# Optimization experiments

Measured on AMD Instinct MI355X. Metric: run time of the kernel, lower is better.

Reference implementation:

```python
import jax, jax.numpy as jnp
import numpy as np
from jax import lax

B, C, H, W = 16, 384, 28, 28
HEADS = 8


def _ln(x, g, b):
    mu = jnp.mean(x, axis=-1, keepdims=True)
    var = jnp.var(x, axis=-1, keepdims=True)
    return (x - mu) * lax.rsqrt(var + 1e-5) * g + b


def setup_inputs() -> dict:
    key = jax.random.key(0)
    ks = jax.random.split(key, 8)
    s = 0.02
    return {
        "cls_token": jax.random.normal(ks[0], (B, 1, C), dtype=jnp.float32),
        "x": jax.random.normal(ks[1], (B, C, H, W), dtype=jnp.float32),
        "conv_w": jax.random.normal(ks[2], (C, 1, 3, 3), dtype=jnp.float32) * s,
        "conv_b": jnp.zeros((C,), jnp.float32),
        "ln1_g": jnp.ones((C,), jnp.float32),
        "ln1_b": jnp.zeros((C,), jnp.float32),
        "qkv_w": jax.random.normal(ks[3], (3 * C, C), dtype=jnp.float32) * s,
        "proj_w": jax.random.normal(ks[4], (C, C), dtype=jnp.float32) * s,
        "proj_b": jnp.zeros((C,), jnp.float32),
        "ln2_g": jnp.ones((C,), jnp.float32),
        "ln2_b": jnp.zeros((C,), jnp.float32),
        "fc1_w": jax.random.normal(ks[5], (4 * C, C), dtype=jnp.float32) * s,
        "fc1_b": jnp.zeros((4 * C,), jnp.float32),
        "fc2_w": jax.random.normal(ks[6], (C, 4 * C), dtype=jnp.float32) * s,
        "fc2_b": jnp.zeros((C,), jnp.float32),
    }


def reference(cls_token, x, conv_w, conv_b, ln1_g, ln1_b, qkv_w, proj_w, proj_b,
              ln2_g, ln2_b, fc1_w, fc1_b, fc2_w, fc2_b):
    Bv, Cv, Hv, Wv = x.shape
    h = HEADS
    d = Cv // h
    # depthwise 3x3 positional conv (groups=dim), residual add
    pe = lax.conv_general_dilated(
        x, conv_w, window_strides=(1, 1), padding="SAME",
        feature_group_count=Cv,
        dimension_numbers=("NCHW", "OIHW", "NCHW")) + conv_b[None, :, None, None]
    x = x + pe
    x_patch = x.reshape(Bv, Cv, Hv * Wv).transpose(0, 2, 1)  # [B, HW, C]
    xc = jnp.concatenate([cls_token, x_patch], axis=1)       # [B, N, C]
    N = xc.shape[1]

    # --- Attention with inline global_attn stats (first-call / int sentinel path) ---
    y = _ln(xc, ln1_g, ln1_b)
    qkv = (y @ qkv_w.T).reshape(Bv, N, 3, h, d)
    q = qkv[:, :, 0].transpose(0, 2, 1, 3)  # [B, h, N, d]
    k = qkv[:, :, 1].transpose(0, 2, 1, 3)
    v = qkv[:, :, 2].transpose(0, 2, 1, 3)
    scale = d ** -0.5
    attn = jax.nn.softmax(jnp.einsum("bhnd,bhmd->bhnm", q, k) * scale, axis=-1)
    # per-token global attention statistic: mean over heads of cls row (excl. cls)
    global_attn = jnp.mean(attn[:, :, 0, 1:], axis=1)  # [B, N-1]
    o = jnp.einsum("bhnm,bhmd->bhnd", attn, v).transpose(0, 2, 1, 3).reshape(Bv, N, Cv)
    xc = xc + (o @ proj_w.T + proj_b)

    # --- MLP (GELU exact, matching torch nn.GELU default) ---
    y2 = _ln(xc, ln2_g, ln2_b)
    m = jax.nn.gelu(y2 @ fc1_w.T + fc1_b, approximate=False) @ fc2_w.T + fc2_b
    xc = xc + m

    cls_out = xc[:, :1]                                            # [B, 1, C]
    x_out = xc[:, 1:].transpose(0, 2, 1).reshape(Bv, Cv, Hv, Wv)    # [B, C, H, W]
    return cls_out, x_out, global_attn
```

## Files before the change

### kernel.cpp

```cpp
#include <hip/hip_runtime.h>
#include <hip/hip_bf16.h>

#define DI __device__ __forceinline__

typedef __attribute__((ext_vector_type(4))) float f32x4;
typedef __attribute__((ext_vector_type(8))) short bf16x8;
typedef __attribute__((ext_vector_type(4))) short bf16x4;

static constexpr int CB = 16;
static constexpr int CC = 384;
static constexpr int CH = 28, CW = 28;
static constexpr int CD = 48;
static constexpr int CN = 785;
static constexpr int CM = CB * CN;
static constexpr int C3 = 3 * CC;
static constexpr int CF = 4 * CC;
static constexpr int HW = CH * CW;
static constexpr int NP = 832;

DI short f2b(float f) {
  __hip_bfloat16 h = __float2bfloat16(f);
  return *reinterpret_cast<short*>(&h);
}
DI float b2f(short s) {
  union { unsigned u; float f; } x;
  x.u = ((unsigned)(unsigned short)s) << 16;
  return x.f;
}

DI void gload16(const short* g, short* l) {
  __builtin_amdgcn_global_load_lds((const __attribute__((address_space(1))) void*)g,
                                   (__attribute__((address_space(3))) void*)l, 16, 0, 0);
}

__global__ void k_misc(const float* __restrict__ cls, float* __restrict__ xc,
                       float* __restrict__ ga) {
  const int gid = blockIdx.x * 256 + threadIdx.x;
  if (gid < CB * HW) ga[gid] = 0.f;
  if (gid < CB * CC) {
    const int b = gid / CC, c = gid % CC;
    xc[((size_t)b * CN) * CC + c] = cls[gid];
  }
}

__global__ void k_wconv(const float* __restrict__ s0, const float* __restrict__ s1,
                        const float* __restrict__ s2, const float* __restrict__ s3,
                        short* __restrict__ dst) {
  const int gid = (blockIdx.x * 256 + threadIdx.x) * 4;
  if (gid >= 1769472) return;
  const float* s; int off;
  if (gid < 442368)       { s = s0; off = gid; }
  else if (gid < 589824)  { s = s1; off = gid - 442368; }
  else if (gid < 1179648) { s = s2; off = gid - 589824; }
  else                    { s = s3; off = gid - 1179648; }
  f32x4 v = *(const f32x4*)(s + off);
  bf16x4 o;
#pragma unroll
  for (int i = 0; i < 4; i++) o[i] = f2b(v[i]);
  *(bf16x4*)(dst + gid) = o;
}

__global__ __launch_bounds__(256) void k_conv_t(const float* __restrict__ x,
                                                const float* __restrict__ cw,
                                                const float* __restrict__ cb,
                                                float* __restrict__ xc) {
  __shared__ float T[64][65];
  __shared__ float Wc[64 * 9];
  __shared__ float Cbs[64];
  const int b = blockIdx.z;
  const int cc = blockIdx.y * 64;
  const int hw0 = blockIdx.x * 64;
  const int t = threadIdx.x;
  const int hwi = t & 63, ci0 = t >> 6;
  const int hw = hw0 + hwi;
  const int yy = hw / CW, xx = hw % CW;
  const int ci2 = t & 63, hb2 = t >> 6;

  for (int i = t; i < 64 * 9; i += 256) Wc[i] = cw[cc * 9 + i];
  if (t < 64) Cbs[t] = cb[cc + t];
  __syncthreads();
  if (hw < HW) {
    const int ctr = yy * CW + xx;
    int off9[9]; float mk9[9];
#pragma unroll
    for (int ky = 0; ky < 3; ky++)
#pragma unroll
      for (int kx = 0; kx < 3; kx++) {
        const int iy = yy + ky - 1, ix = xx + kx - 1;
        const bool v = (iy >= 0 && iy < CH && ix >= 0 && ix < CW);
        off9[ky * 3 + kx] = v ? iy * CW + ix : ctr;
        mk9[ky * 3 + kx] = v ? 1.f : 0.f;
      }
#pragma unroll
    for (int j = 0; j < 16; j += 2) {
      const int cl0 = ci0 * 16 + j;
      const float* xp0 = x + ((size_t)(b * CC + cc + cl0)) * HW;
      const float* xp1 = xp0 + HW;
      float t0[9], t1[9];
#pragma unroll
      for (int q = 0; q < 9; q++) { t0[q] = xp0[off9[q]]; t1[q] = xp1[off9[q]]; }
      const float c0 = xp0[ctr], c1 = xp1[ctr];
      float a0 = Cbs[cl0], a1 = Cbs[cl0 + 1];
#pragma unroll
      for (int q = 0; q < 9; q++) {
        a0 += Wc[cl0 * 9 + q] * (t0[q] * mk9[q]);
        a1 += Wc[(cl0 + 1) * 9 + q] * (t1[q] * mk9[q]);
      }
      T[cl0][hwi] = c0 + a0;
      T[cl0 + 1][hwi] = c1 + a1;
    }
  }
  __syncthreads();
#pragma unroll
  for (int j = 0; j < 16; j++) {
    const int hwl = hb2 + j * 4;
    if (hw0 + hwl < HW)
      xc[((size_t)b * CN + 1 + hw0 + hwl) * CC + cc + ci2] = T[ci2][hwl];
  }
}

__global__ __launch_bounds__(256) void k_ln(const float* __restrict__ xin,
                                            const float* __restrict__ g,
                                            const float* __restrict__ bta,
                                            short* __restrict__ y, int Mtot) {
  const int row = blockIdx.x * 4 + (threadIdx.x >> 6);
  const int l = threadIdx.x & 63;
  if (row >= Mtot) return;
  const float* xr = xin + (size_t)row * CC;
  float v[6], s = 0.f, ss = 0.f;
#pragma unroll
  for (int i = 0; i < 6; i++) {
    v[i] = xr[l + i * 64];
    s += v[i];
    ss += v[i] * v[i];
  }
#pragma unroll
  for (int m = 1; m < 64; m <<= 1) { s += __shfl_xor(s, m); ss += __shfl_xor(ss, m); }
  const float mu = s * (1.f / CC);
  const float var = ss * (1.f / CC) - mu * mu;
  const float r = rsqrtf(var + 1e-5f);
#pragma unroll
  for (int i = 0; i < 6; i++) {
    const int c = l + i * 64;
    y[(size_t)row * CC + c] = f2b((v[i] - mu) * r * g[c] + bta[c]);
  }
}

template <int BM, int DOGELU, int DORES, int DOBIAS, int OUTBF>
__global__ __launch_bounds__(256) void k_gemm(const short* __restrict__ A,
                                              const short* __restrict__ W,
                                              const float* __restrict__ bias,
                                              const float* __restrict__ resid,
                                              void* __restrict__ out_,
                                              int M, int N, int K) {
  constexpr int MI = BM / 32;
  constexpr int ACALLS = BM / 64;
  constexpr int ASZ = BM * 32, BSZ = 128 * 32;
  __shared__ short As[3 * ASZ];
  __shared__ short Bs[3 * BSZ];
  const int bm = blockIdx.x * BM, bn = blockIdx.y * 128;
  const int t = threadIdx.x, w = t >> 6, l = t & 63, g = l >> 4, li = l & 15;
  const int wm = (w >> 1) * (BM / 2), wn = (w & 1) * 64;

  const int srow = l >> 2;
  const int scol = (l & 3) * 8;
  const short* aSrc[ACALLS]; int aOff[ACALLS];
#pragma unroll
  for (int j = 0; j < ACALLS; j++) {
    int arow = bm + w * (BM / 4) + j * 16 + srow; if (arow > M - 1) arow = M - 1;
    aSrc[j] = A + (size_t)arow * K + scol;
    aOff[j] = (w * (BM / 4) + j * 16) * 32;
  }
  const short* bSrc[2]; int bOff[2];
#pragma unroll
  for (int j = 0; j < 2; j++) {
    const int brow = bn + w * 32 + j * 16 + srow;
    bSrc[j] = W + (size_t)brow * K + scol;
    bOff[j] = (w * 32 + j * 16) * 32;
  }

  auto stage = [&](int buf, int kt) {
    const int ko = kt * 32;
#pragma unroll
    for (int j = 0; j < ACALLS; j++)
      gload16(aSrc[j] + ko, &As[buf * ASZ] + aOff[j]);
#pragma unroll
    for (int j = 0; j < 2; j++)
      gload16(bSrc[j] + ko, &Bs[buf * BSZ] + bOff[j]);
  };

  f32x4 acc[MI][4] = {};
  const int nkt = K / 32;
  stage(0, 0);
  stage(1, 1);
  int cur = 0;
  for (int kt = 0; kt < nkt; kt++) {
    if (kt + 2 < nkt) {
      int nb = cur + 2; if (nb >= 3) nb -= 3;
      stage(nb, kt + 2);
      if constexpr (BM == 128) asm volatile("s_waitcnt vmcnt(8)" ::: "memory");
      else                     asm volatile("s_waitcnt vmcnt(6)" ::: "memory");
    } else if (kt + 2 == nkt) {
      if constexpr (BM == 128) asm volatile("s_waitcnt vmcnt(4)" ::: "memory");
      else                     asm volatile("s_waitcnt vmcnt(3)" ::: "memory");
    } else {
      asm volatile("s_waitcnt vmcnt(0)" ::: "memory");
    }
    __builtin_amdgcn_sched_barrier(0);
    __builtin_amdgcn_s_barrier();

    const short* Ab = &As[cur * ASZ];
    const short* Bb = &Bs[cur * BSZ];
    bf16x8 af[MI], bf[4];
#pragma unroll
    for (int mi = 0; mi < MI; mi++)
      af[mi] = *(const bf16x8*)&Ab[(wm + mi * 16 + li) * 32 + g * 8];
#pragma unroll
    for (int ni = 0; ni < 4; ni++)
      bf[ni] = *(const bf16x8*)&Bb[(wn + ni * 16 + li) * 32 + g * 8];
#pragma unroll
    for (int mi = 0; mi < MI; mi++)
#pragma unroll
      for (int ni = 0; ni < 4; ni++)
        acc[mi][ni] = __builtin_amdgcn_mfma_f32_16x16x32_bf16(af[mi], bf[ni], acc[mi][ni], 0, 0, 0);

    asm volatile("s_waitcnt lgkmcnt(0)" ::: "memory");
    __builtin_amdgcn_sched_barrier(0);
    __builtin_amdgcn_s_barrier();
    cur = (cur == 2) ? 0 : cur + 1;
  }

#pragma unroll
  for (int mi = 0; mi < MI; mi++)
#pragma unroll
    for (int ni = 0; ni < 4; ni++) {
      const int col = bn + wn + ni * 16 + li;
      float bv = 0.f;
      if constexpr (DOBIAS) bv = bias[col];
#pragma unroll
      for (int r = 0; r < 4; r++) {
        const int row = bm + wm + mi * 16 + g * 4 + r;
        if (row < M) {
          float v = acc[mi][ni][r] + bv;
          if constexpr (DOGELU) v = 0.5f * v * (1.f + erff(v * 0.7071067811865475f));
          if constexpr (DORES) v += resid[(size_t)row * N + col];
          if constexpr (OUTBF)
            ((short*)out_)[(size_t)row * N + col] = f2b(v);
          else
            ((float*)out_)[(size_t)row * N + col] = v;
        }
      }
    }
}

__global__ __launch_bounds__(256) void k_vt(const short* __restrict__ qkv,
                                            short* __restrict__ vt) {
  __shared__ short Tl[48 * 71];
  const int n0 = blockIdx.x * 64;
  const int bh = blockIdx.y;
  const int b = bh >> 3, h = bh & 7;
  const int t = threadIdx.x;
  const size_t bbase = (size_t)b * CN;
#pragma unroll
  for (int it = 0; it < 2; it++) {
    const int gi = t + it * 256;
    if (gi < 384) {
      const int nrel = gi / 6, dg = gi % 6;
      const int n = n0 + nrel;
      bf16x8 val = {};
      if (n < CN)
        val = *(const bf16x8*)(qkv + (bbase + n) * C3 + 2 * CC + h * CD + dg * 8);
#pragma unroll
      for (int i = 0; i < 8; i++) Tl[(dg * 8 + i) * 71 + nrel] = val[i];
    }
  }
  __syncthreads();
#pragma unroll
  for (int it = 0; it < 2; it++) {
    const int gj = t + it * 256;
    if (gj < 384) {
      const int d = gj >> 3, ng = gj & 7;
      bf16x8 v;
#pragma unroll
      for (int i = 0; i < 8; i++) v[i] = Tl[d * 71 + ng * 8 + i];
      *(bf16x8*)(vt + ((size_t)bh * CD + d) * NP + n0 + ng * 8) = v;
    }
  }
}

__global__ __launch_bounds__(256) void k_attn(const short* __restrict__ qkv,
                                              const short* __restrict__ vt,
                                              short* __restrict__ o) {
  __shared__ short Ks[64 * 48];
  __shared__ short Vs[48 * 64];
  const int f = blockIdx.x;
  const int xslot = f & 7, grp = f >> 3;
  const int bh = xslot + 8 * (grp & 15);
  const int qt = grp >> 4;
  const int b = bh >> 3, h = bh & 7;
  const int q0 = qt * 64;
  const int t = threadIdx.x, w = t >> 6, l = t & 63, g = l >> 4, li = l & 15;
  const size_t bbase = (size_t)b * CN;

  const int qrow = q0 + w * 16 + li;
  const int qr = qrow > CN - 1 ? CN - 1 : qrow;
  const short* qb = qkv + (bbase + qr) * C3 + h * CD;
  bf16x8 qf0 = *(const bf16x8*)(qb + g * 8);
  bf16x8 qf1 = {};
  if (g < 2) qf1 = *(const bf16x8*)(qb + 32 + g * 8);

  float mr = -1e30f, ls = 0.f;
  f32x4 oa[3] = {};
  const float scale = 0.14433756729740643f;

  const int krow0 = t / 6, kcg0 = t % 6;
  const int krow1 = (t + 256) / 6, kcg1 = (t + 256) % 6;
  const int vd0 = t >> 3, vkvg0 = t & 7;
  const int vd1 = (t + 256) >> 3, vkvg1 = (t + 256) & 7;
  const short* kbase = qkv + bbase * C3 + CC + h * CD;
  const short* vbase = vt + (size_t)bh * CD * NP;

  bf16x8 kr0 = {}, kr1 = {}, vr0 = {}, vr1 = {};
  kr0 = *(const bf16x8*)(kbase + (size_t)min(krow0, CN - 1) * C3 + kcg0 * 8);
  vr0 = *(const bf16x8*)(vbase + vd0 * NP + vkvg0 * 8);
  if (t < 128) {
    kr1 = *(const bf16x8*)(kbase + (size_t)min(krow1, CN - 1) * C3 + kcg1 * 8);
    vr1 = *(const bf16x8*)(vbase + vd1 * NP + vkvg1 * 8);
  }

  for (int kt = 0; kt < 13; kt++) {
    const int kv0 = kt * 64;
    __syncthreads();
    *(bf16x8*)((char*)Ks + ((krow0 * 96 + kcg0 * 16) ^ ((krow0 & 7) << 4))) = kr0;
    *(bf16x8*)((char*)Vs + ((vd0 * 128 + vkvg0 * 16) ^ ((vd0 & 7) << 4))) = vr0;
    if (t < 128) {
      *(bf16x8*)((char*)Ks + ((krow1 * 96 + kcg1 * 16) ^ ((krow1 & 7) << 4))) = kr1;
      *(bf16x8*)((char*)Vs + ((vd1 * 128 + vkvg1 * 16) ^ ((vd1 & 7) << 4))) = vr1;
    }
    __syncthreads();
    if (kt < 12) {
      const int kn = kv0 + 64;
      kr0 = *(const bf16x8*)(kbase + (size_t)min(kn + krow0, CN - 1) * C3 + kcg0 * 8);
      vr0 = *(const bf16x8*)(vbase + vd0 * NP + kn + vkvg0 * 8);
      if (t < 128) {
        kr1 = *(const bf16x8*)(kbase + (size_t)min(kn + krow1, CN - 1) * C3 + kcg1 * 8);
        vr1 = *(const bf16x8*)(vbase + vd1 * NP + kn + vkvg1 * 8);
      }
    }

    f32x4 s[4];
    __builtin_amdgcn_s_setprio(1);
#pragma unroll
    for (int ni = 0; ni < 4; ni++) {
      const int krw = ni * 16 + li;
      const int sw = (krw & 7) << 4;
      bf16x8 kf0 = *(const bf16x8*)((char*)Ks + ((krw * 96 + g * 16) ^ sw));
      bf16x8 kf1 = {};
      if (g < 2) kf1 = *(const bf16x8*)((char*)Ks + ((krw * 96 + 64 + g * 16) ^ sw));
      f32x4 acc = {};
      acc = __builtin_amdgcn_mfma_f32_16x16x32_bf16(kf0, qf0, acc, 0, 0, 0);
      acc = __builtin_amdgcn_mfma_f32_16x16x32_bf16(kf1, qf1, acc, 0, 0, 0);
      s[ni] = acc;
    }
    __builtin_amdgcn_s_setprio(0);

    float mt = -1e30f;
#pragma unroll
    for (int ni = 0; ni < 4; ni++)
#pragma unroll
      for (int r = 0; r < 4; r++) {
        const int kva = kv0 + ni * 16 + g * 4 + r;
        const float v = (kva < CN) ? s[ni][r] * scale : -1e30f;
        s[ni][r] = v;
        mt = fmaxf(mt, v);
      }
    mt = fmaxf(mt, __shfl_xor(mt, 16));
    mt = fmaxf(mt, __shfl_xor(mt, 32));
    const float mn = fmaxf(mr, mt);
    const float al = __expf(mr - mn);
    mr = mn;
    float ps = 0.f;
#pragma unroll
    for (int ni = 0; ni < 4; ni++)
#pragma unroll
      for (int r = 0; r < 4; r++) {
        const float p = __expf(s[ni][r] - mn);
        s[ni][r] = p;
        ps += p;
      }
    ps += __shfl_xor(ps, 16);
    ps += __shfl_xor(ps, 32);
    ls = ls * al + ps;

    const int sb = (l & 48) + ((l & 48) >> 2);
    float ar[4];
#pragma unroll
    for (int r = 0; r < 4; r++) ar[r] = __shfl(al, sb + r);
#pragma unroll
    for (int d = 0; d < 3; d++)
#pragma unroll
      for (int r = 0; r < 4; r++) oa[d][r] *= ar[r];

    bf16x8 pa[2];
#pragma unroll
    for (int ks = 0; ks < 2; ks++)
#pragma unroll
      for (int i = 0; i < 8; i++)
        pa[ks][i] = f2b(i < 4 ? s[2 * ks][i] : s[2 * ks + 1][i - 4]);

    __builtin_amdgcn_s_setprio(1);
#pragma unroll
    for (int d = 0; d < 3; d++) {
      const int drow = d * 16 + li;
      const int sw = (drow & 7) << 4;
#pragma unroll
      for (int ks = 0; ks < 2; ks++) {
        bf16x4 lo = *(const bf16x4*)((char*)Vs + ((drow * 128 + ks * 64 + g * 8) ^ sw));
        bf16x4 hi = *(const bf16x4*)((char*)Vs + ((drow * 128 + ks * 64 + 32 + g * 8) ^ sw));
        bf16x8 vb;
#pragma unroll
        for (int i = 0; i < 4; i++) { vb[i] = lo[i]; vb[4 + i] = hi[i]; }
        oa[d] = __builtin_amdgcn_mfma_f32_16x16x32_bf16(pa[ks], vb, oa[d], 0, 0, 0);
      }
    }
    __builtin_amdgcn_s_setprio(0);
  }

  const int sb = (l & 48) + ((l & 48) >> 2);
  float lr[4];
#pragma unroll
  for (int r = 0; r < 4; r++) lr[r] = __shfl(ls, sb + r);
#pragma unroll
  for (int d = 0; d < 3; d++)
#pragma unroll
    for (int r = 0; r < 4; r++) {
      const int n = q0 + w * 16 + g * 4 + r;
      if (n < CN)
        o[(bbase + n) * CC + h * CD + d * 16 + li] = f2b(oa[d][r] / lr[r]);
    }
}

__global__ __launch_bounds__(256) void k_gattn(const short* __restrict__ qkv,
                                               float* __restrict__ ga) {
  const int b = blockIdx.x >> 3, h = blockIdx.x & 7;
  __shared__ float red[4];
  const int t = threadIdx.x;
  const size_t bbase = (size_t)b * CN;
  const short* q0 = qkv + bbase * C3 + h * CD;
  float qv[CD];
#pragma unroll
  for (int i = 0; i < CD; i++) qv[i] = b2f(q0[i]);
  float lg[4], ev[4];
  float lmax = -1e30f;
#pragma unroll
  for (int j = 0; j < 4; j++) {
    const int m = t + j * 256;
    if (m < CN) {
      const short* kr = qkv + (bbase + m) * C3 + CC + h * CD;
      float acc = 0.f;
#pragma unroll
      for (int i = 0; i < CD; i++) acc += qv[i] * b2f(kr[i]);
      lg[j] = acc * 0.14433756729740643f;
      lmax = fmaxf(lmax, lg[j]);
    } else lg[j] = -1e30f;
  }
  for (int msk = 1; msk < 64; msk <<= 1) lmax = fmaxf(lmax, __shfl_xor(lmax, msk));
  if ((t & 63) == 0) red[t >> 6] = lmax;
  __syncthreads();
  lmax = fmaxf(fmaxf(red[0], red[1]), fmaxf(red[2], red[3]));
  __syncthreads();
  float es = 0.f;
#pragma unroll
  for (int j = 0; j < 4; j++) {
    ev[j] = (t + j * 256 < CN) ? __expf(lg[j] - lmax) : 0.f;
    es += ev[j];
  }
  for (int msk = 1; msk < 64; msk <<= 1) es += __shfl_xor(es, msk);
  if ((t & 63) == 0) red[t >> 6] = es;
  __syncthreads();
  es = red[0] + red[1] + red[2] + red[3];
  const float inv = 0.125f / es;
#pragma unroll
  for (int j = 0; j < 4; j++) {
    const int m = t + j * 256;
    if (m >= 1 && m < CN) atomicAdd(&ga[b * HW + m - 1], ev[j] * inv);
  }
}

__global__ __launch_bounds__(256) void k_out(const float* __restrict__ xc,
                                             float* __restrict__ outp) {
  const int b = blockIdx.y, tile = blockIdx.x, t = threadIdx.x;
  if (tile == 78) {
    for (int i = t; i < CC; i += 256)
      outp[b * CC + i] = xc[((size_t)b * CN) * CC + i];
    return;
  }
  __shared__ float T[64][65];
  const int ct = tile / 13, ht = tile % 13;
  const int c0 = ct * 64, hw0 = ht * 64;
  const int ci = t & 63, hb = t >> 6;
  for (int j = 0; j < 16; j++) {
    const int hwl = hb + j * 4;
    if (hw0 + hwl < HW)
      T[ci][hwl] = xc[((size_t)b * CN + 1 + hw0 + hwl) * CC + c0 + ci];
  }
  __syncthreads();
  const int hi = t & 63, cb2 = t >> 6;
  float* xo = outp + CB * CC;
  for (int j = 0; j < 16; j++) {
    const int cl = cb2 + j * 4;
    if (hw0 + hi < HW)
      xo[((size_t)(b * CC + c0 + cl)) * HW + hw0 + hi] = T[cl][hi];
  }
}

extern "C" void kernel_launch(void* const* d_in, const int* in_sizes, int n_in,
                              void* d_out, int out_size, void* d_ws, size_t ws_size,
                              hipStream_t stream) {
  const float* cls    = (const float*)d_in[0];
  const float* x      = (const float*)d_in[1];
  const float* conv_w = (const float*)d_in[2];
  const float* conv_b = (const float*)d_in[3];
  const float* ln1_g  = (const float*)d_in[4];
  const float* ln1_b  = (const float*)d_in[5];
  const float* qkv_w  = (const float*)d_in[6];
  const float* proj_w = (const float*)d_in[7];
  const float* proj_b = (const float*)d_in[8];
  const float* ln2_g  = (const float*)d_in[9];
  const float* ln2_b  = (const float*)d_in[10];
  const float* fc1_w  = (const float*)d_in[11];
  const float* fc1_b  = (const float*)d_in[12];
  const float* fc2_w  = (const float*)d_in[13];
  const float* fc2_b  = (const float*)d_in[14];

  float* outf = (float*)d_out;
  float* ga = outf + (size_t)CB * CC + (size_t)CB * CC * HW;
  short* vtb = (short*)(outf + CB * CC);

  char* ws = (char*)d_ws;
  float* xc   = (float*)ws;
  short* y    = (short*)(ws + 19292160ULL);
  short* qkvb = (short*)(ws + 28938240ULL);
  short* o    = (short*)(ws + 57876480ULL);
  short* m1   = (short*)(ws + 28938240ULL);
  short* wbuf = (short*)(ws + 67522560ULL);
  short* qkv_wb = wbuf;
  short* proj_wb = wbuf + 442368;
  short* fc1_wb  = wbuf + 589824;
  short* fc2_wb  = wbuf + 1179648;

  const int thr = 256;
  k_misc<<<49, thr, 0, stream>>>(cls, xc, ga);
  k_wconv<<<1728, thr, 0, stream>>>(qkv_w, proj_w, fc1_w, fc2_w, wbuf);
  k_conv_t<<<dim3(13, 6, CB), thr, 0, stream>>>(x, conv_w, conv_b, xc);
  k_ln<<<CM / 4, thr, 0, stream>>>(xc, ln1_g, ln1_b, y, CM);
  k_gemm<128, 0, 0, 0, 1><<<dim3(99, C3 / 128), thr, 0, stream>>>(
      y, qkv_wb, nullptr, nullptr, qkvb, CM, C3, CC);
  k_vt<<<dim3(13, CB * 8), thr, 0, stream>>>(qkvb, vtb);
  k_attn<<<1664, thr, 0, stream>>>(qkvb, vtb, o);
  k_gattn<<<CB * 8, thr, 0, stream>>>(qkvb, ga);
  k_gemm<64, 0, 1, 1, 0><<<dim3(197, CC / 128), thr, 0, stream>>>(
      o, proj_wb, proj_b, xc, xc, CM, CC, CC);
  k_ln<<<CM / 4, thr, 0, stream>>>(xc, ln2_g, ln2_b, y, CM);
  k_gemm<128, 1, 0, 1, 1><<<dim3(99, CF / 128), thr, 0, stream>>>(
      y, fc1_wb, fc1_b, nullptr, m1, CM, CF, CC);
  k_gemm<64, 0, 1, 1, 0><<<dim3(197, CC / 128), thr, 0, stream>>>(
      m1, fc2_wb, fc2_b, xc, xc, CM, CC, CF);
  k_out<<<dim3(79, CB), thr, 0, stream>>>(xc, outf);
}
```

Baseline: 351.0 us.

## Remap GEMM workgroups across XCDs and switch to double-buffered LDS pipeline

The GEMM kernel now launches a 1D grid and remaps block IDs so that consecutive logical tiles (row-major over N tiles) land on the same XCD chiplet, which is meant to improve L2 reuse of A rows and weight tiles. The pipeline also drops from three LDS buffers with explicit vmcnt waits to a simple two-buffer scheme synchronized by __syncthreads. That cuts LDS use and may raise occupancy, but it gives less prefetch depth and relies on the compiler's conservative waitcnts, which could expose load latency.

```diff
diff --git a/kernel.cpp b/kernel.cpp
--- a/kernel.cpp
+++ b/kernel.cpp
@@ -152,13 +152,20 @@
                                               const float* __restrict__ bias,
                                               const float* __restrict__ resid,
                                               void* __restrict__ out_,
-                                              int M, int N, int K) {
+                                              int M, int N, int K, int NN) {
   constexpr int MI = BM / 32;
   constexpr int ACALLS = BM / 64;
   constexpr int ASZ = BM * 32, BSZ = 128 * 32;
-  __shared__ short As[3 * ASZ];
-  __shared__ short Bs[3 * BSZ];
-  const int bm = blockIdx.x * BM, bn = blockIdx.y * 128;
+  __shared__ short As[2 * ASZ];
+  __shared__ short Bs[2 * BSZ];
+
+  const int nwg = gridDim.x;
+  const int q = nwg >> 3, r = nwg & 7;
+  const int x = blockIdx.x & 7, j = blockIdx.x >> 3;
+  const int base = (x < r) ? x * (q + 1) : r * (q + 1) + (x - r) * q;
+  const int wgid = base + j;
+  const int bm = (wgid / NN) * BM, bn = (wgid % NN) * 128;
+
   const int t = threadIdx.x, w = t >> 6, l = t & 63, g = l >> 4, li = l & 15;
   const int wm = (w >> 1) * (BM / 2), wn = (w & 1) * 64;
 
@@ -166,49 +173,36 @@
   const int scol = (l & 3) * 8;
   const short* aSrc[ACALLS]; int aOff[ACALLS];
 #pragma unroll
-  for (int j = 0; j < ACALLS; j++) {
-    int arow = bm + w * (BM / 4) + j * 16 + srow; if (arow > M - 1) arow = M - 1;
-    aSrc[j] = A + (size_t)arow * K + scol;
-    aOff[j] = (w * (BM / 4) + j * 16) * 32;
+  for (int jj = 0; jj < ACALLS; jj++) {
+    int arow = bm + w * (BM / 4) + jj * 16 + srow; if (arow > M - 1) arow = M - 1;
+    aSrc[jj] = A + (size_t)arow * K + scol;
+    aOff[jj] = (w * (BM / 4) + jj * 16) * 32;
   }
   const short* bSrc[2]; int bOff[2];
 #pragma unroll
-  for (int j = 0; j < 2; j++) {
-    const int brow = bn + w * 32 + j * 16 + srow;
-    bSrc[j] = W + (size_t)brow * K + scol;
-    bOff[j] = (w * 32 + j * 16) * 32;
+  for (int jj = 0; jj < 2; jj++) {
+    const int brow = bn + w * 32 + jj * 16 + srow;
+    bSrc[jj] = W + (size_t)brow * K + scol;
+    bOff[jj] = (w * 32 + jj * 16) * 32;
   }
 
   auto stage = [&](int buf, int kt) {
     const int ko = kt * 32;
 #pragma unroll
-    for (int j = 0; j < ACALLS; j++)
-      gload16(aSrc[j] + ko, &As[buf * ASZ] + aOff[j]);
-#pragma unroll
-    for (int j = 0; j < 2; j++)
-      gload16(bSrc[j] + ko, &Bs[buf * BSZ] + bOff[j]);
+    for (int jj = 0; jj < ACALLS; jj++)
+      gload16(aSrc[jj] + ko, &As[buf * ASZ] + aOff[jj]);
+#pragma unroll
+    for (int jj = 0; jj < 2; jj++)
+      gload16(bSrc[jj] + ko, &Bs[buf * BSZ] + bOff[jj]);
   };
 
   f32x4 acc[MI][4] = {};
   const int nkt = K / 32;
   stage(0, 0);
-  stage(1, 1);
+  __syncthreads();
   int cur = 0;
   for (int kt = 0; kt < nkt; kt++) {
-    if (kt + 2 < nkt) {
-      int nb = cur + 2; if (nb >= 3) nb -= 3;
-      stage(nb, kt + 2);
-      if constexpr (BM == 128) asm volatile("s_waitcnt vmcnt(8)" ::: "memory");
-      else                     asm volatile("s_waitcnt vmcnt(6)" ::: "memory");
-    } else if (kt + 2 == nkt) {
-      if constexpr (BM == 128) asm volatile("s_waitcnt vmcnt(4)" ::: "memory");
-      else                     asm volatile("s_waitcnt vmcnt(3)" ::: "memory");
-    } else {
-      asm volatile("s_waitcnt vmcnt(0)" ::: "memory");
-    }
-    __builtin_amdgcn_sched_barrier(0);
-    __builtin_amdgcn_s_barrier();
-
+    if (kt + 1 < nkt) stage(cur ^ 1, kt + 1);
     const short* Ab = &As[cur * ASZ];
     const short* Bb = &Bs[cur * BSZ];
     bf16x8 af[MI], bf[4];
@@ -223,11 +217,8 @@
 #pragma unroll
       for (int ni = 0; ni < 4; ni++)
         acc[mi][ni] = __builtin_amdgcn_mfma_f32_16x16x32_bf16(af[mi], bf[ni], acc[mi][ni], 0, 0, 0);
-
-    asm volatile("s_waitcnt lgkmcnt(0)" ::: "memory");
-    __builtin_amdgcn_sched_barrier(0);
-    __builtin_amdgcn_s_barrier();
-    cur = (cur == 2) ? 0 : cur + 1;
+    __syncthreads();
+    cur ^= 1;
   }
 
 #pragma unroll
@@ -238,10 +229,10 @@
       float bv = 0.f;
       if constexpr (DOBIAS) bv = bias[col];
 #pragma unroll
-      for (int r = 0; r < 4; r++) {
-        const int row = bm + wm + mi * 16 + g * 4 + r;
+      for (int rr = 0; rr < 4; rr++) {
+        const int row = bm + wm + mi * 16 + g * 4 + rr;
         if (row < M) {
-          float v = acc[mi][ni][r] + bv;
+          float v = acc[mi][ni][rr] + bv;
           if constexpr (DOGELU) v = 0.5f * v * (1.f + erff(v * 0.7071067811865475f));
           if constexpr (DORES) v += resid[(size_t)row * N + col];
           if constexpr (OUTBF)
@@ -368,10 +359,10 @@
 #pragma unroll
     for (int ni = 0; ni < 4; ni++)
 #pragma unroll
-      for (int r = 0; r < 4; r++) {
-        const int kva = kv0 + ni * 16 + g * 4 + r;
-        const float v = (kva < CN) ? s[ni][r] * scale : -1e30f;
-        s[ni][r] = v;
+      for (int rr = 0; rr < 4; rr++) {
+        const int kva = kv0 + ni * 16 + g * 4 + rr;
+        const float v = (kva < CN) ? s[ni][rr] * scale : -1e30f;
+        s[ni][rr] = v;
         mt = fmaxf(mt, v);
       }
     mt = fmaxf(mt, __shfl_xor(mt, 16));
@@ -383,9 +374,9 @@
 #pragma unroll
     for (int ni = 0; ni < 4; ni++)
 #pragma unroll
-      for (int r = 0; r < 4; r++) {
-        const float p = __expf(s[ni][r] - mn);
-        s[ni][r] = p;
+      for (int rr = 0; rr < 4; rr++) {
+        const float p = __expf(s[ni][rr] - mn);
+        s[ni][rr] = p;
         ps += p;
       }
     ps += __shfl_xor(ps, 16);
@@ -395,11 +386,11 @@
     const int sb = (l & 48) + ((l & 48) >> 2);
     float ar[4];
 #pragma unroll
-    for (int r = 0; r < 4; r++) ar[r] = __shfl(al, sb + r);
+    for (int rr = 0; rr < 4; rr++) ar[rr] = __shfl(al, sb + rr);
 #pragma unroll
     for (int d = 0; d < 3; d++)
 #pragma unroll
-      for (int r = 0; r < 4; r++) oa[d][r] *= ar[r];
+      for (int rr = 0; rr < 4; rr++) oa[d][rr] *= ar[rr];
 
     bf16x8 pa[2];
 #pragma unroll
@@ -429,14 +420,14 @@
   const int sb = (l & 48) + ((l & 48) >> 2);
   float lr[4];
 #pragma unroll
-  for (int r = 0; r < 4; r++) lr[r] = __shfl(ls, sb + r);
+  for (int rr = 0; rr < 4; rr++) lr[rr] = __shfl(ls, sb + rr);
 #pragma unroll
   for (int d = 0; d < 3; d++)
 #pragma unroll
-    for (int r = 0; r < 4; r++) {
-      const int n = q0 + w * 16 + g * 4 + r;
+    for (int rr = 0; rr < 4; rr++) {
+      const int n = q0 + w * 16 + g * 4 + rr;
       if (n < CN)
-        o[(bbase + n) * CC + h * CD + d * 16 + li] = f2b(oa[d][r] / lr[r]);
+        o[(bbase + n) * CC + h * CD + d * 16 + li] = f2b(oa[d][rr] / lr[rr]);
     }
 }
 
@@ -554,17 +545,17 @@
   k_wconv<<<1728, thr, 0, stream>>>(qkv_w, proj_w, fc1_w, fc2_w, wbuf);
   k_conv_t<<<dim3(13, 6, CB), thr, 0, stream>>>(x, conv_w, conv_b, xc);
   k_ln<<<CM / 4, thr, 0, stream>>>(xc, ln1_g, ln1_b, y, CM);
-  k_gemm<128, 0, 0, 0, 1><<<dim3(99, C3 / 128), thr, 0, stream>>>(
-      y, qkv_wb, nullptr, nullptr, qkvb, CM, C3, CC);
+  k_gemm<128, 0, 0, 0, 1><<<99 * 9, thr, 0, stream>>>(
+      y, qkv_wb, nullptr, nullptr, qkvb, CM, C3, CC, 9);
   k_vt<<<dim3(13, CB * 8), thr, 0, stream>>>(qkvb, vtb);
   k_attn<<<1664, thr, 0, stream>>>(qkvb, vtb, o);
   k_gattn<<<CB * 8, thr, 0, stream>>>(qkvb, ga);
-  k_gemm<64, 0, 1, 1, 0><<<dim3(197, CC / 128), thr, 0, stream>>>(
-      o, proj_wb, proj_b, xc, xc, CM, CC, CC);
+  k_gemm<64, 0, 1, 1, 0><<<197 * 3, thr, 0, stream>>>(
+      o, proj_wb, proj_b, xc, xc, CM, CC, CC, 3);
   k_ln<<<CM / 4, thr, 0, stream>>>(xc, ln2_g, ln2_b, y, CM);
-  k_gemm<128, 1, 0, 1, 1><<<dim3(99, CF / 128), thr, 0, stream>>>(
-      y, fc1_wb, fc1_b, nullptr, m1, CM, CF, CC);
-  k_gemm<64, 0, 1, 1, 0><<<dim3(197, CC / 128), thr, 0, stream>>>(
-      m1, fc2_wb, fc2_b, xc, xc, CM, CC, CF);
+  k_gemm<128, 1, 0, 1, 1><<<99 * 12, thr, 0, stream>>>(
+      y, fc1_wb, fc1_b, nullptr, m1, CM, CF, CC, 12);
+  k_gemm<64, 0, 1, 1, 0><<<197 * 3, thr, 0, stream>>>(
+      m1, fc2_wb, fc2_b, xc, xc, CM, CC, CF, 3);
   k_out<<<dim3(79, CB), thr, 0, stream>>>(xc, outf);
 }
```

Result: faster. 325.9 us (-7.2%).
